# Optimization experiments

Measured on AMD Instinct MI355X. Metric: run time of the kernel, lower is better.

The kernel has to match this reference:

```python
import jax, jax.numpy as jnp
import numpy as np

K = 16
D_MODEL = 128

def _gather(pts, idx):
    # pts: [B,N,C], idx: [B,N,K] -> [B,N,K,C]
    return jax.vmap(lambda p, i: p[i])(pts, idx)

def setup_inputs() -> dict:
    key = jax.random.key(0)
    ks = jax.random.split(key, 20)
    s = 0.05
    def w(k_, shape):
        return jax.random.normal(k_, shape, dtype=jnp.float32) * s
    B, N, C = 4, 4096, 3
    TF, D = 128, D_MODEL
    return {
        "xyz": jax.random.normal(ks[0], (B, N, C), dtype=jnp.float32),
        "W0a": w(ks[1], (C, TF)),  "b0a": jnp.zeros((TF,), jnp.float32),
        "W0b": w(ks[2], (TF, TF)), "b0b": jnp.zeros((TF,), jnp.float32),
        "W1":  w(ks[3], (TF, D)),  "b1":  jnp.zeros((D,), jnp.float32),
        "W2":  w(ks[4], (D, TF)),  "b2":  jnp.zeros((TF,), jnp.float32),
        "Wd1": w(ks[5], (C, D)),   "bd1": jnp.zeros((D,), jnp.float32),
        "Wd2": w(ks[6], (D, D)),   "bd2": jnp.zeros((D,), jnp.float32),
        "Wg1": w(ks[7], (D, D)),   "bg1": jnp.zeros((D,), jnp.float32),
        "Wg2": w(ks[8], (D, D)),   "bg2": jnp.zeros((D,), jnp.float32),
        "Wq":  w(ks[9], (D, D)),
        "Wk":  w(ks[10], (D, D)),
        "Wv":  w(ks[11], (D, D)),
    }

def reference(xyz, W0a, b0a, W0b, b0b, W1, b1, W2, b2,
              Wd1, bd1, Wd2, bd2, Wg1, bg1, Wg2, bg2, Wq, Wk, Wv):
    sq = jnp.sum(xyz * xyz, axis=-1)
    dists = sq[:, :, None] - 2.0 * jnp.einsum('bnc,bmc->bnm', xyz, xyz) + sq[:, None, :]
    _, knn_idx = jax.lax.top_k(-dists, K)          # [B,N,K] nearest neighbors

    knn_xyz = _gather(xyz, knn_idx)                # [B,N,K,3]
    features = jax.nn.relu(xyz @ W0a + b0a) @ W0b + b0b   # fc0  [B,N,TF]
    pre = features
    x = features @ W1 + b1                          # fc1  [B,N,D]
    q = x @ Wq                                      # [B,N,D]
    kf = _gather(x @ Wk, knn_idx)                   # [B,N,K,D]
    vf = _gather(x @ Wv, knn_idx)                   # [B,N,K,D]

    delta = xyz[:, :, None, :] - knn_xyz            # [B,N,K,3]
    pos_enc = jax.nn.relu(delta @ Wd1 + bd1) @ Wd2 + bd2   # fc_delta [B,N,K,D]

    h = q[:, :, None, :] - kf + pos_enc
    attn_logits = jax.nn.relu(h @ Wg1 + bg1) @ Wg2 + bg2   # fc_gamma [B,N,K,D]
    attn = jax.nn.softmax(attn_logits / np.sqrt(D_MODEL).astype(np.float32), axis=-2)

    res = jnp.einsum('bmnf,bmnf->bmf', attn, vf + pos_enc)  # [B,N,D]
    res = res @ W2 + b2 + pre                               # [B,N,TF]
    return res, attn
```

## Files before the change

kernel.cpp:

```cpp
#include <hip/hip_runtime.h>
#include <math.h>

#define BB 4
#define NN 4096
#define KNNK 16
#define DD 128
#define BN (BB*NN)

typedef __attribute__((ext_vector_type(8))) short short8;
typedef __attribute__((ext_vector_type(4))) float floatx4;

__device__ __forceinline__ short f2bf(float x) {
  unsigned u = __float_as_uint(x);
  unsigned r = (u + 0x7fffu + ((u >> 16) & 1u)) >> 16;
  return (short)r;
}

__device__ __forceinline__ float bf2f(short h) {
  return __uint_as_float((unsigned)(unsigned short)h << 16);
}

__device__ __forceinline__ void split_from_lds(const float* __restrict__ trans,
                                               int c, int g, short8 ah[4],
                                               short8 al[4]) {
#pragma unroll
  for (int s = 0; s < 4; ++s) {
    const float* p_ = &trans[c * 132 + s * 32 + g * 8];
    float4 u0 = *reinterpret_cast<const float4*>(p_);
    float4 u1 = *reinterpret_cast<const float4*>(p_ + 4);
    float tmp[8] = {u0.x, u0.y, u0.z, u0.w, u1.x, u1.y, u1.z, u1.w};
#pragma unroll
    for (int j = 0; j < 8; ++j) {
      short h_ = f2bf(tmp[j]);
      ah[s][j] = h_;
      al[s][j] = f2bf(tmp[j] - bf2f(h_));
    }
  }
}

__device__ __forceinline__ void split_gemm2(const short* __restrict__ Bh,
                                            int nt0, int lane,
                                            const short8 ah[4],
                                            const short8 al[4], floatx4& acc0,
                                            floatx4& acc1) {
  const short* Bl = Bh + 16384;
#pragma unroll
  for (int ks = 0; ks < 4; ++ks) {
    const size_t o0 = ((size_t)((nt0 + 0) * 4 + ks) * 64 + lane) * 8;
    const size_t o1 = ((size_t)((nt0 + 1) * 4 + ks) * 64 + lane) * 8;
    short8 bh0 = *reinterpret_cast<const short8*>(Bh + o0);
    short8 bl0 = *reinterpret_cast<const short8*>(Bl + o0);
    short8 bh1 = *reinterpret_cast<const short8*>(Bh + o1);
    short8 bl1 = *reinterpret_cast<const short8*>(Bl + o1);
    acc0 = __builtin_amdgcn_mfma_f32_16x16x32_bf16(ah[ks], bh0, acc0, 0, 0, 0);
    acc1 = __builtin_amdgcn_mfma_f32_16x16x32_bf16(ah[ks], bh1, acc1, 0, 0, 0);
    acc0 = __builtin_amdgcn_mfma_f32_16x16x32_bf16(ah[ks], bl0, acc0, 0, 0, 0);
    acc1 = __builtin_amdgcn_mfma_f32_16x16x32_bf16(ah[ks], bl1, acc1, 0, 0, 0);
    acc0 = __builtin_amdgcn_mfma_f32_16x16x32_bf16(al[ks], bh0, acc0, 0, 0, 0);
    acc1 = __builtin_amdgcn_mfma_f32_16x16x32_bf16(al[ks], bh1, acc1, 0, 0, 0);
  }
}

__device__ __forceinline__ void ced(double& a, double& b) {
  double mn = fmin(a, b);
  double mx = fmax(a, b);
  a = mn;
  b = mx;
}

__device__ __forceinline__ void dsort16(double v[16]) {
#define CE(i, j) ced(v[i], v[j]);
  CE(0, 1) CE(2, 3) CE(4, 5) CE(6, 7) CE(8, 9) CE(10, 11) CE(12, 13) CE(14, 15)
  CE(0, 2) CE(1, 3) CE(4, 6) CE(5, 7) CE(8, 10) CE(9, 11) CE(12, 14) CE(13, 15)
  CE(1, 2) CE(5, 6) CE(9, 10) CE(13, 14)
  CE(0, 4) CE(1, 5) CE(2, 6) CE(3, 7) CE(8, 12) CE(9, 13) CE(10, 14) CE(11, 15)
  CE(2, 4) CE(3, 5) CE(10, 12) CE(11, 13)
  CE(1, 2) CE(3, 4) CE(5, 6) CE(9, 10) CE(11, 12) CE(13, 14)
  CE(0, 8) CE(1, 9) CE(2, 10) CE(3, 11) CE(4, 12) CE(5, 13) CE(6, 14) CE(7, 15)
  CE(4, 8) CE(5, 9) CE(6, 10) CE(7, 11)
  CE(2, 4) CE(3, 5) CE(6, 8) CE(7, 9) CE(10, 12) CE(11, 13)
  CE(1, 2) CE(3, 4) CE(5, 6) CE(7, 8) CE(9, 10) CE(11, 12) CE(13, 14)
#undef CE
}

__device__ __forceinline__ void dbitonic16(double m[16]) {
#pragma unroll
  for (int s = 8; s >= 1; s >>= 1) {
#pragma unroll
    for (int i = 0; i < 16; ++i) {
      if ((i & s) == 0) ced(m[i], m[i + s]);
    }
  }
}

__global__ __launch_bounds__(256, 4) void knn_kernel(const float* __restrict__ xyz,
                                                     int* __restrict__ knn) {
  const int wv = threadIdx.x >> 6;
  const int lane = threadIdx.x & 63;
  const int q = blockIdx.x * 4 + wv;
  const int b = q >> 12;
  const int n = q & 4095;
  const float* xb = xyz + (size_t)b * NN * 3;

  const float qx = xb[n * 3 + 0], qy = xb[n * 3 + 1], qz = xb[n * 3 + 2];
  const float qsq = __fadd_rn(__fadd_rn(__fmul_rn(qx, qx), __fmul_rn(qy, qy)),
                              __fmul_rn(qz, qz));

  double top[16];
#pragma unroll
  for (int batch = 0; batch < 4; ++batch) {
    double v[16];
#pragma unroll
    for (int i = 0; i < 16; ++i) {
      const int c = (batch * 16 + i) * 64 + lane;
      float cx = xb[c * 3 + 0], cy = xb[c * 3 + 1], cz = xb[c * 3 + 2];
      float csq = __fadd_rn(__fadd_rn(__fmul_rn(cx, cx), __fmul_rn(cy, cy)),
                            __fmul_rn(cz, cz));
      float dot = __fadd_rn(__fadd_rn(__fmul_rn(qx, cx), __fmul_rn(qy, cy)),
                            __fmul_rn(qz, cz));
      float d = __fadd_rn(__fsub_rn(qsq, __fmul_rn(2.0f, dot)), csq);
      unsigned u = __float_as_uint(d);
      u = (u & 0x80000000u) ? ~u : (u | 0x80000000u);
      unsigned long long key =
          0x3FF0000000000000ULL | (((unsigned long long)u << 12) | (unsigned)c);
      v[i] = __longlong_as_double((long long)key);
    }
    dsort16(v);
    if (batch == 0) {
#pragma unroll
      for (int i = 0; i < 16; ++i) top[i] = v[i];
    } else {
      double m[16];
#pragma unroll
      for (int i = 0; i < 16; ++i)
        m[i] = fmin(top[i], v[15 - i]);
      dbitonic16(m);
#pragma unroll
      for (int i = 0; i < 16; ++i) top[i] = m[i];
    }
  }

#pragma unroll
  for (int mask = 1; mask <= 32; mask <<= 1) {
    double oth[16];
#pragma unroll
    for (int i = 0; i < 16; ++i) {
      double y = __shfl_xor(top[15 - i], mask);
      oth[i] = fmin(y, top[i]);
    }
    dbitonic16(oth);
#pragma unroll
    for (int i = 0; i < 16; ++i) top[i] = oth[i];
  }

  if (lane == 0) {
    int* outp = knn + (size_t)q * KNNK;
#pragma unroll
    for (int k = 0; k < 16; ++k)
      outp[k] = (int)(__double_as_longlong(top[k]) & 0xFFFLL);
  }
}

__global__ void swz_all_kernel(const float* __restrict__ Wd2,
                               const float* __restrict__ Wg1,
                               const float* __restrict__ Wg2,
                               const float* __restrict__ W0b,
                               const float* __restrict__ W1,
                               const float* __restrict__ Wq,
                               const float* __restrict__ Wk,
                               const float* __restrict__ Wv,
                               const float* __restrict__ W2,
                               short* __restrict__ wsw,
                               short* __restrict__ wsplit) {
  int t = blockIdx.x * 256 + threadIdx.x;
  if (t < 3 * 2048) {
    int stage = t / 2048;
    int rem = t % 2048;
    int nt = rem / 256;
    int ks = (rem % 256) / 64;
    int lane = rem % 64;
    const float* W = (stage == 0) ? Wd2 : (stage == 1) ? Wg1 : Wg2;
    short8 o;
#pragma unroll
    for (int j = 0; j < 8; ++j) {
      int k = ks * 32 + (lane >> 4) * 8 + j;
      int n = nt * 16 + (lane & 15);
      o[j] = f2bf(W[k * 128 + n]);
    }
    *reinterpret_cast<short8*>(wsw + (size_t)t * 8) = o;
  } else {
    int u = t - 3 * 2048;
    if (u >= 6 * 2048) return;
    int mat = u / 2048;
    int rem = u % 2048;
    int nt = rem / 256;
    int ks = (rem % 256) / 64;
    int lane = rem % 64;
    const float* W = (mat == 0) ? W0b : (mat == 1) ? W1 : (mat == 2) ? Wq
                     : (mat == 3) ? Wk : (mat == 4) ? Wv : W2;
    short8 hi, lo;
#pragma unroll
    for (int j = 0; j < 8; ++j) {
      int k = ks * 32 + (lane >> 4) * 8 + j;
      int n = nt * 16 + (lane & 15);
      float w = W[k * 128 + n];
      short h = f2bf(w);
      hi[j] = h;
      lo[j] = f2bf(w - bf2f(h));
    }
    *reinterpret_cast<short8*>(wsplit + ((size_t)(2 * mat) * 2048 + rem) * 8) = hi;
    *reinterpret_cast<short8*>(wsplit + ((size_t)(2 * mat + 1) * 2048 + rem) * 8) = lo;
  }
}

__global__ __launch_bounds__(256, 4) void point_mlp_mfma_kernel(
    const float* __restrict__ xyz, const float* __restrict__ W0a,
    const float* __restrict__ b0a, const float* __restrict__ b0b,
    const float* __restrict__ b1, const short* __restrict__ wsplit,
    float* __restrict__ pre, float* __restrict__ qv, float* __restrict__ kv,
    float* __restrict__ vv) {
  const int wv = threadIdx.x >> 6;
  const int lane = threadIdx.x & 63;
  const int g = lane >> 4;
  const int c = lane & 15;
  const int g0 = blockIdx.x * 16;
  const int nt0 = wv * 2;

  __shared__ __attribute__((aligned(16))) float trans[16 * 132];
  __shared__ float xs[64];
  if (threadIdx.x < 48) {
    int p = threadIdx.x / 3, cc = threadIdx.x % 3;
    xs[p * 4 + cc] = xyz[(size_t)(g0 + p) * 3 + cc];
  }
  __syncthreads();

  short8 ah[4], al[4];
  {
    const float x0 = xs[c * 4 + 0], x1 = xs[c * 4 + 1], x2 = xs[c * 4 + 2];
#pragma unroll
    for (int s = 0; s < 4; ++s) {
#pragma unroll
      for (int j = 0; j < 8; ++j) {
        const int k = s * 32 + g * 8 + j;
        float v = fmaf(x2, W0a[256 + k],
                       fmaf(x1, W0a[128 + k], fmaf(x0, W0a[k], b0a[k])));
        v = fmaxf(v, 0.f);
        const short h = f2bf(v);
        ah[s][j] = h;
        al[s][j] = f2bf(v - bf2f(h));
      }
    }
  }

  floatx4 acc0, acc1;
  const floatx4 zf = (floatx4){0.f, 0.f, 0.f, 0.f};

  acc0 = zf; acc1 = zf;
  split_gemm2(wsplit + 0 * 32768, nt0, lane, ah, al, acc0, acc1);
  {
    const float bb0 = b0b[nt0 * 16 + c];
    const float bb1 = b0b[(nt0 + 1) * 16 + c];
#pragma unroll
    for (int r = 0; r < 4; ++r) {
      const int row = g * 4 + r;
      float v0 = acc0[r] + bb0;
      float v1 = acc1[r] + bb1;
      pre[(size_t)(g0 + row) * 128 + nt0 * 16 + c] = v0;
      pre[(size_t)(g0 + row) * 128 + (nt0 + 1) * 16 + c] = v1;
      trans[row * 132 + nt0 * 16 + c] = v0;
      trans[row * 132 + (nt0 + 1) * 16 + c] = v1;
    }
  }
  __syncthreads();
  split_from_lds(trans, c, g, ah, al);
  __syncthreads();

  acc0 = zf; acc1 = zf;
  split_gemm2(wsplit + 1 * 32768, nt0, lane, ah, al, acc0, acc1);
  {
    const float bb0 = b1[nt0 * 16 + c];
    const float bb1 = b1[(nt0 + 1) * 16 + c];
#pragma unroll
    for (int r = 0; r < 4; ++r) {
      const int row = g * 4 + r;
      trans[row * 132 + nt0 * 16 + c] = acc0[r] + bb0;
      trans[row * 132 + (nt0 + 1) * 16 + c] = acc1[r] + bb1;
    }
  }
  __syncthreads();
  split_from_lds(trans, c, g, ah, al);
  __syncthreads();

#define GSTORE(dst)                                                            \
  _Pragma("unroll") for (int r = 0; r < 4; ++r) {                              \
    const int row = g0 + g * 4 + r;                                            \
    dst[(size_t)row * 128 + nt0 * 16 + c] = acc0[r];                           \
    dst[(size_t)row * 128 + (nt0 + 1) * 16 + c] = acc1[r];                     \
  }

  acc0 = zf; acc1 = zf;
  split_gemm2(wsplit + 2 * 32768, nt0, lane, ah, al, acc0, acc1);
  GSTORE(qv);

  acc0 = zf; acc1 = zf;
  split_gemm2(wsplit + 3 * 32768, nt0, lane, ah, al, acc0, acc1);
  GSTORE(kv);

  acc0 = zf; acc1 = zf;
  split_gemm2(wsplit + 4 * 32768, nt0, lane, ah, al, acc0, acc1);
  GSTORE(vv);

#undef GSTORE
}

__global__ __launch_bounds__(256, 4) void attn_mfma_kernel(
    const float* __restrict__ xyz, const int* __restrict__ knn,
    const float* __restrict__ qv, const float* __restrict__ kv,
    const float* __restrict__ vv, const short* __restrict__ wsw,
    const float* __restrict__ Wd1, const float* __restrict__ bd1,
    const float* __restrict__ bd2, const float* __restrict__ bg1,
    const float* __restrict__ bg2, float* __restrict__ res_ws,
    float* __restrict__ out_attn) {
  const int wv = threadIdx.x >> 6;
  const int lane = threadIdx.x & 63;
  const int g = lane >> 4;
  const int c = lane & 15;
  const int bn = blockIdx.x * 4 + wv;
  const int b = bn >> 12;
  const int base_n = b << 12;

  __shared__ __attribute__((aligned(16))) short conv[4][16 * 136];

  const int* knnp = knn + (size_t)bn * 16;
  const int idxn = knnp[c];
  int idxr[4];
#pragma unroll
  for (int r = 0; r < 4; ++r) idxr[r] = knnp[g * 4 + r];

  float kvf[8][4];
#pragma unroll
  for (int nt = 0; nt < 8; ++nt)
#pragma unroll
    for (int r = 0; r < 4; ++r)
      kvf[nt][r] = kv[((size_t)(base_n + idxr[r])) * 128 + nt * 16 + c];

  const float ddx = xyz[(size_t)bn * 3 + 0] - xyz[((size_t)(base_n + idxn)) * 3 + 0];
  const float ddy = xyz[(size_t)bn * 3 + 1] - xyz[((size_t)(base_n + idxn)) * 3 + 1];
  const float ddz = xyz[(size_t)bn * 3 + 2] - xyz[((size_t)(base_n + idxn)) * 3 + 2];

  short8 af[4];
#pragma unroll
  for (int s = 0; s < 4; ++s) {
#pragma unroll
    for (int j = 0; j < 8; ++j) {
      int d = s * 32 + g * 8 + j;
      float v = fmaf(ddz, Wd1[256 + d],
                     fmaf(ddy, Wd1[128 + d], fmaf(ddx, Wd1[d], bd1[d])));
      af[s][j] = f2bf(fmaxf(v, 0.f));
    }
  }

  float qc[8], bd2v[8];
#pragma unroll
  for (int nt = 0; nt < 8; ++nt) {
    qc[nt] = qv[(size_t)bn * 128 + nt * 16 + c];
    bd2v[nt] = bd2[nt * 16 + c];
  }

  floatx4 acc[8];

#pragma unroll
  for (int nt = 0; nt < 8; ++nt) acc[nt] = (floatx4){0.f, 0.f, 0.f, 0.f};
  {
    const short* Wst = wsw;
#pragma unroll
    for (int ks = 0; ks < 4; ++ks) {
#pragma unroll
      for (int nt = 0; nt < 8; ++nt) {
        short8 bf = *reinterpret_cast<const short8*>(
            Wst + ((size_t)(nt * 4 + ks) * 64 + lane) * 8);
        acc[nt] = __builtin_amdgcn_mfma_f32_16x16x32_bf16(af[ks], bf, acc[nt],
                                                          0, 0, 0);
      }
    }
  }

  float PE[8][4];
#pragma unroll
  for (int nt = 0; nt < 8; ++nt) {
#pragma unroll
    for (int r = 0; r < 4; ++r) {
      float pe = acc[nt][r] + bd2v[nt];
      PE[nt][r] = pe;
      conv[wv][(g * 4 + r) * 136 + nt * 16 + c] =
          f2bf(qc[nt] - kvf[nt][r] + pe);
    }
  }
  __syncthreads();
#pragma unroll
  for (int s = 0; s < 4; ++s)
    af[s] = *reinterpret_cast<const short8*>(&conv[wv][c * 136 + s * 32 + g * 8]);
  __syncthreads();

#pragma unroll
  for (int nt = 0; nt < 8; ++nt) acc[nt] = (floatx4){0.f, 0.f, 0.f, 0.f};
  {
    const short* Wst = wsw + 16384;
#pragma unroll
    for (int ks = 0; ks < 4; ++ks) {
#pragma unroll
      for (int nt = 0; nt < 8; ++nt) {
        short8 bf = *reinterpret_cast<const short8*>(
            Wst + ((size_t)(nt * 4 + ks) * 64 + lane) * 8);
        acc[nt] = __builtin_amdgcn_mfma_f32_16x16x32_bf16(af[ks], bf, acc[nt],
                                                          0, 0, 0);
      }
    }
  }
#pragma unroll
  for (int nt = 0; nt < 8; ++nt) {
    const float bg1v = bg1[nt * 16 + c];
#pragma unroll
    for (int r = 0; r < 4; ++r) {
      conv[wv][(g * 4 + r) * 136 + nt * 16 + c] =
          f2bf(fmaxf(acc[nt][r] + bg1v, 0.f));
    }
  }
  __syncthreads();
#pragma unroll
  for (int s = 0; s < 4; ++s)
    af[s] = *reinterpret_cast<const short8*>(&conv[wv][c * 136 + s * 32 + g * 8]);
  __syncthreads();

#pragma unroll
  for (int nt = 0; nt < 8; ++nt) acc[nt] = (floatx4){0.f, 0.f, 0.f, 0.f};
  {
    const short* Wst = wsw + 32768;
#pragma unroll
    for (int ks = 0; ks < 4; ++ks) {
#pragma unroll
      for (int nt = 0; nt < 8; ++nt) {
        short8 bf = *reinterpret_cast<const short8*>(
            Wst + ((size_t)(nt * 4 + ks) * 64 + lane) * 8);
        acc[nt] = __builtin_amdgcn_mfma_f32_16x16x32_bf16(af[ks], bf, acc[nt],
                                                          0, 0, 0);
      }
    }
  }

  const float inv = 0.0883883476483184f;
  float resv[8];
#pragma unroll
  for (int nt = 0; nt < 8; ++nt) {
    const float bg2v = bg2[nt * 16 + c];
    float l0 = (acc[nt][0] + bg2v) * inv;
    float l1 = (acc[nt][1] + bg2v) * inv;
    float l2 = (acc[nt][2] + bg2v) * inv;
    float l3 = (acc[nt][3] + bg2v) * inv;
    float m4 = fmaxf(fmaxf(l0, l1), fmaxf(l2, l3));
    m4 = fmaxf(m4, __shfl_xor(m4, 16));
    m4 = fmaxf(m4, __shfl_xor(m4, 32));
    float e0 = expf(l0 - m4), e1 = expf(l1 - m4);
    float e2 = expf(l2 - m4), e3 = expf(l3 - m4);
    float s4 = e0 + e1 + e2 + e3;
    s4 += __shfl_xor(s4, 16);
    s4 += __shfl_xor(s4, 32);
    float rs = 1.f / s4;
    float a0 = e0 * rs, a1 = e1 * rs, a2 = e2 * rs, a3 = e3 * rs;
    size_t base = ((size_t)bn * 16 + g * 4) * 128 + nt * 16 + c;
    out_attn[base + 0 * 128] = a0;
    out_attn[base + 1 * 128] = a1;
    out_attn[base + 2 * 128] = a2;
    out_attn[base + 3 * 128] = a3;
    float r = 0.f;
    {
      float v0 = vv[((size_t)(base_n + idxr[0])) * 128 + nt * 16 + c];
      float v1 = vv[((size_t)(base_n + idxr[1])) * 128 + nt * 16 + c];
      float v2 = vv[((size_t)(base_n + idxr[2])) * 128 + nt * 16 + c];
      float v3 = vv[((size_t)(base_n + idxr[3])) * 128 + nt * 16 + c];
      r = fmaf(a0, v0 + PE[nt][0], r);
      r = fmaf(a1, v1 + PE[nt][1], r);
      r = fmaf(a2, v2 + PE[nt][2], r);
      r = fmaf(a3, v3 + PE[nt][3], r);
    }
    r += __shfl_xor(r, 16);
    r += __shfl_xor(r, 32);
    resv[nt] = r;
  }
  if (g == 0) {
#pragma unroll
    for (int nt = 0; nt < 8; ++nt)
      res_ws[(size_t)bn * 128 + nt * 16 + c] = resv[nt];
  }
}

__global__ __launch_bounds__(256, 4) void epilogue_mfma_kernel(
    const float* __restrict__ res_ws, const short* __restrict__ wsplit,
    const float* __restrict__ b2, const float* __restrict__ pre,
    float* __restrict__ out_res) {
  const int wv = threadIdx.x >> 6;
  const int lane = threadIdx.x & 63;
  const int g = lane >> 4;
  const int c = lane & 15;
  const int g0 = blockIdx.x * 16;
  const int nt0 = wv * 2;

  __shared__ __attribute__((aligned(16))) float trans[16 * 132];

#pragma unroll
  for (int i = 0; i < 2; ++i) {
    int idx4 = threadIdx.x + i * 256;
    int row = idx4 >> 5;
    int col4 = idx4 & 31;
    float4 v = *reinterpret_cast<const float4*>(
        res_ws + (size_t)(g0 + row) * 128 + col4 * 4);
    *reinterpret_cast<float4*>(&trans[row * 132 + col4 * 4]) = v;
  }
  __syncthreads();

  short8 ah[4], al[4];
  split_from_lds(trans, c, g, ah, al);

  float prv0[4], prv1[4];
  const float bb0 = b2[nt0 * 16 + c];
  const float bb1 = b2[(nt0 + 1) * 16 + c];
#pragma unroll
  for (int r = 0; r < 4; ++r) {
    prv0[r] = pre[(size_t)(g0 + g * 4 + r) * 128 + nt0 * 16 + c];
    prv1[r] = pre[(size_t)(g0 + g * 4 + r) * 128 + (nt0 + 1) * 16 + c];
  }

  floatx4 acc0 = (floatx4){0.f, 0.f, 0.f, 0.f};
  floatx4 acc1 = (floatx4){0.f, 0.f, 0.f, 0.f};
  split_gemm2(wsplit + 5 * 32768, nt0, lane, ah, al, acc0, acc1);

#pragma unroll
  for (int r = 0; r < 4; ++r) {
    const int row = g0 + g * 4 + r;
    out_res[(size_t)row * 128 + nt0 * 16 + c] = acc0[r] + bb0 + prv0[r];
    out_res[(size_t)row * 128 + (nt0 + 1) * 16 + c] = acc1[r] + bb1 + prv1[r];
  }
}

extern "C" void kernel_launch(void* const* d_in, const int* in_sizes, int n_in,
                              void* d_out, int out_size, void* d_ws,
                              size_t ws_size, hipStream_t stream) {
  const float* xyz = (const float*)d_in[0];
  const float* W0a = (const float*)d_in[1];
  const float* b0a = (const float*)d_in[2];
  const float* W0b = (const float*)d_in[3];
  const float* b0b = (const float*)d_in[4];
  const float* W1 = (const float*)d_in[5];
  const float* b1 = (const float*)d_in[6];
  const float* W2 = (const float*)d_in[7];
  const float* b2 = (const float*)d_in[8];
  const float* Wd1 = (const float*)d_in[9];
  const float* bd1 = (const float*)d_in[10];
  const float* Wd2 = (const float*)d_in[11];
  const float* bd2 = (const float*)d_in[12];
  const float* Wg1 = (const float*)d_in[13];
  const float* bg1 = (const float*)d_in[14];
  const float* Wg2 = (const float*)d_in[15];
  const float* bg2 = (const float*)d_in[16];
  const float* Wq = (const float*)d_in[17];
  const float* Wk = (const float*)d_in[18];
  const float* Wv = (const float*)d_in[19];

  char* ws = (char*)d_ws;
  int* knn = (int*)ws;
  float* pre = (float*)(ws + (1 << 20));
  float* qv = (float*)(ws + (9 << 20));
  float* kv = (float*)(ws + (17 << 20));
  float* vv = (float*)(ws + (25 << 20));
  float* res_ws = (float*)(ws + (33 << 20));
  short* wsw = (short*)(ws + (41 << 20));
  short* wsplit = (short*)(ws + (41 << 20) + (128 << 10));

  float* out_res = (float*)d_out;
  float* out_attn = out_res + (size_t)BN * DD;

  hipLaunchKernelGGL(swz_all_kernel, dim3(72), dim3(256), 0, stream, Wd2, Wg1,
                     Wg2, W0b, W1, Wq, Wk, Wv, W2, wsw, wsplit);
  hipLaunchKernelGGL(knn_kernel, dim3(4096), dim3(256), 0, stream, xyz, knn);
  hipLaunchKernelGGL(point_mlp_mfma_kernel, dim3(1024), dim3(256), 0, stream,
                     xyz, W0a, b0a, b0b, b1, wsplit, pre, qv, kv, vv);
  hipLaunchKernelGGL(attn_mfma_kernel, dim3(4096), dim3(256), 0, stream, xyz,
                     knn, qv, kv, vv, wsw, Wd1, bd1, bd2, bg1, bg2, res_ws,
                     out_attn);
  hipLaunchKernelGGL(epilogue_mfma_kernel, dim3(1024), dim3(256), 0, stream,
                     res_ws, wsplit, b2, pre, out_res);
}
```

Baseline: 381.0 us.

## Replace block barriers with per-wave LDS fences and batch weight loads in MFMA stages

Swaps the __syncthreads around the per-wave conv staging buffer for an lgkmcnt wait, since each wave only touches its own LDS slice. Groups the B-fragment loads four at a time ahead of the MFMAs in each GEMM stage. Splits the last GEMM and softmax into two halves, prefetching the gathered V values before the MFMAs so global latency overlaps compute. The aim is to cut block-wide stalls and expose more memory-level parallelism. In return it leans on the assumption that the LDS regions are wave-private, and it raises register pressure.

```diff
diff --git a/kernel.cpp b/kernel.cpp
--- a/kernel.cpp
+++ b/kernel.cpp
@@ -19,6 +19,8 @@
 __device__ __forceinline__ float bf2f(short h) {
   return __uint_as_float((unsigned)(unsigned short)h << 16);
 }
+
+#define LDSFENCE() asm volatile("s_waitcnt lgkmcnt(0)" ::: "memory")
 
 __device__ __forceinline__ void split_from_lds(const float* __restrict__ trans,
                                                int c, int g, short8 ah[4],
@@ -369,21 +371,25 @@
 
   floatx4 acc[8];
 
+#define STAGE_GEMM(WOFF)                                                       \
+  {                                                                            \
+    const short* Wst = wsw + (WOFF);                                           \
+    _Pragma("unroll") for (int ks = 0; ks < 4; ++ks) {                         \
+      _Pragma("unroll") for (int h2 = 0; h2 < 2; ++h2) {                       \
+        short8 bfr[4];                                                         \
+        _Pragma("unroll") for (int i = 0; i < 4; ++i)                          \
+          bfr[i] = *reinterpret_cast<const short8*>(                           \
+              Wst + ((size_t)((h2 * 4 + i) * 4 + ks) * 64 + lane) * 8);        \
+        _Pragma("unroll") for (int i = 0; i < 4; ++i)                          \
+          acc[h2 * 4 + i] = __builtin_amdgcn_mfma_f32_16x16x32_bf16(           \
+              af[ks], bfr[i], acc[h2 * 4 + i], 0, 0, 0);                       \
+      }                                                                        \
+    }                                                                          \
+  }
+
 #pragma unroll
   for (int nt = 0; nt < 8; ++nt) acc[nt] = (floatx4){0.f, 0.f, 0.f, 0.f};
-  {
-    const short* Wst = wsw;
-#pragma unroll
-    for (int ks = 0; ks < 4; ++ks) {
-#pragma unroll
-      for (int nt = 0; nt < 8; ++nt) {
-        short8 bf = *reinterpret_cast<const short8*>(
-            Wst + ((size_t)(nt * 4 + ks) * 64 + lane) * 8);
-        acc[nt] = __builtin_amdgcn_mfma_f32_16x16x32_bf16(af[ks], bf, acc[nt],
-                                                          0, 0, 0);
-      }
-    }
-  }
+  STAGE_GEMM(0);
 
   float PE[8][4];
 #pragma unroll
@@ -396,27 +402,14 @@
           f2bf(qc[nt] - kvf[nt][r] + pe);
     }
   }
-  __syncthreads();
+  LDSFENCE();
 #pragma unroll
   for (int s = 0; s < 4; ++s)
     af[s] = *reinterpret_cast<const short8*>(&conv[wv][c * 136 + s * 32 + g * 8]);
-  __syncthreads();
 
 #pragma unroll
   for (int nt = 0; nt < 8; ++nt) acc[nt] = (floatx4){0.f, 0.f, 0.f, 0.f};
-  {
-    const short* Wst = wsw + 16384;
-#pragma unroll
-    for (int ks = 0; ks < 4; ++ks) {
-#pragma unroll
-      for (int nt = 0; nt < 8; ++nt) {
-        short8 bf = *reinterpret_cast<const short8*>(
-            Wst + ((size_t)(nt * 4 + ks) * 64 + lane) * 8);
-        acc[nt] = __builtin_amdgcn_mfma_f32_16x16x32_bf16(af[ks], bf, acc[nt],
-                                                          0, 0, 0);
-      }
-    }
-  }
+  STAGE_GEMM(16384);
 #pragma unroll
   for (int nt = 0; nt < 8; ++nt) {
     const float bg1v = bg1[nt * 16 + c];
@@ -426,67 +419,78 @@
           f2bf(fmaxf(acc[nt][r] + bg1v, 0.f));
     }
   }
-  __syncthreads();
+  LDSFENCE();
 #pragma unroll
   for (int s = 0; s < 4; ++s)
     af[s] = *reinterpret_cast<const short8*>(&conv[wv][c * 136 + s * 32 + g * 8]);
-  __syncthreads();
-
-#pragma unroll
-  for (int nt = 0; nt < 8; ++nt) acc[nt] = (floatx4){0.f, 0.f, 0.f, 0.f};
-  {
-    const short* Wst = wsw + 32768;
-#pragma unroll
-    for (int ks = 0; ks < 4; ++ks) {
-#pragma unroll
-      for (int nt = 0; nt < 8; ++nt) {
-        short8 bf = *reinterpret_cast<const short8*>(
-            Wst + ((size_t)(nt * 4 + ks) * 64 + lane) * 8);
-        acc[nt] = __builtin_amdgcn_mfma_f32_16x16x32_bf16(af[ks], bf, acc[nt],
-                                                          0, 0, 0);
-      }
-    }
-  }
 
   const float inv = 0.0883883476483184f;
   float resv[8];
 #pragma unroll
-  for (int nt = 0; nt < 8; ++nt) {
-    const float bg2v = bg2[nt * 16 + c];
-    float l0 = (acc[nt][0] + bg2v) * inv;
-    float l1 = (acc[nt][1] + bg2v) * inv;
-    float l2 = (acc[nt][2] + bg2v) * inv;
-    float l3 = (acc[nt][3] + bg2v) * inv;
-    float m4 = fmaxf(fmaxf(l0, l1), fmaxf(l2, l3));
-    m4 = fmaxf(m4, __shfl_xor(m4, 16));
-    m4 = fmaxf(m4, __shfl_xor(m4, 32));
-    float e0 = expf(l0 - m4), e1 = expf(l1 - m4);
-    float e2 = expf(l2 - m4), e3 = expf(l3 - m4);
-    float s4 = e0 + e1 + e2 + e3;
-    s4 += __shfl_xor(s4, 16);
-    s4 += __shfl_xor(s4, 32);
-    float rs = 1.f / s4;
-    float a0 = e0 * rs, a1 = e1 * rs, a2 = e2 * rs, a3 = e3 * rs;
-    size_t base = ((size_t)bn * 16 + g * 4) * 128 + nt * 16 + c;
-    out_attn[base + 0 * 128] = a0;
-    out_attn[base + 1 * 128] = a1;
-    out_attn[base + 2 * 128] = a2;
-    out_attn[base + 3 * 128] = a3;
-    float r = 0.f;
+  for (int h = 0; h < 2; ++h) {
+    const int ntb = h * 4;
+    float vvf[4][4];
+#pragma unroll
+    for (int i = 0; i < 4; ++i)
+#pragma unroll
+      for (int r = 0; r < 4; ++r)
+        vvf[i][r] =
+            vv[((size_t)(base_n + idxr[r])) * 128 + (ntb + i) * 16 + c];
+
+    floatx4 acch[4];
+#pragma unroll
+    for (int i = 0; i < 4; ++i) acch[i] = (floatx4){0.f, 0.f, 0.f, 0.f};
     {
-      float v0 = vv[((size_t)(base_n + idxr[0])) * 128 + nt * 16 + c];
-      float v1 = vv[((size_t)(base_n + idxr[1])) * 128 + nt * 16 + c];
-      float v2 = vv[((size_t)(base_n + idxr[2])) * 128 + nt * 16 + c];
-      float v3 = vv[((size_t)(base_n + idxr[3])) * 128 + nt * 16 + c];
-      r = fmaf(a0, v0 + PE[nt][0], r);
-      r = fmaf(a1, v1 + PE[nt][1], r);
-      r = fmaf(a2, v2 + PE[nt][2], r);
-      r = fmaf(a3, v3 + PE[nt][3], r);
-    }
-    r += __shfl_xor(r, 16);
-    r += __shfl_xor(r, 32);
-    resv[nt] = r;
-  }
+      const short* Wst = wsw + 32768;
+#pragma unroll
+      for (int ks = 0; ks < 4; ++ks) {
+        short8 bfr[4];
+#pragma unroll
+        for (int i = 0; i < 4; ++i)
+          bfr[i] = *reinterpret_cast<const short8*>(
+              Wst + ((size_t)((ntb + i) * 4 + ks) * 64 + lane) * 8);
+#pragma unroll
+        for (int i = 0; i < 4; ++i)
+          acch[i] = __builtin_amdgcn_mfma_f32_16x16x32_bf16(af[ks], bfr[i],
+                                                            acch[i], 0, 0, 0);
+      }
+    }
+
+#pragma unroll
+    for (int i = 0; i < 4; ++i) {
+      const int nt = ntb + i;
+      const float bg2v = bg2[nt * 16 + c];
+      float l0 = (acch[i][0] + bg2v) * inv;
+      float l1 = (acch[i][1] + bg2v) * inv;
+      float l2 = (acch[i][2] + bg2v) * inv;
+      float l3 = (acch[i][3] + bg2v) * inv;
+      float m4 = fmaxf(fmaxf(l0, l1), fmaxf(l2, l3));
+      m4 = fmaxf(m4, __shfl_xor(m4, 16));
+      m4 = fmaxf(m4, __shfl_xor(m4, 32));
+      float e0 = expf(l0 - m4), e1 = expf(l1 - m4);
+      float e2 = expf(l2 - m4), e3 = expf(l3 - m4);
+      float s4 = e0 + e1 + e2 + e3;
+      s4 += __shfl_xor(s4, 16);
+      s4 += __shfl_xor(s4, 32);
+      float rs = 1.f / s4;
+      float a0 = e0 * rs, a1 = e1 * rs, a2 = e2 * rs, a3 = e3 * rs;
+      size_t base = ((size_t)bn * 16 + g * 4) * 128 + nt * 16 + c;
+      out_attn[base + 0 * 128] = a0;
+      out_attn[base + 1 * 128] = a1;
+      out_attn[base + 2 * 128] = a2;
+      out_attn[base + 3 * 128] = a3;
+      float r = 0.f;
+      r = fmaf(a0, vvf[i][0] + PE[nt][0], r);
+      r = fmaf(a1, vvf[i][1] + PE[nt][1], r);
+      r = fmaf(a2, vvf[i][2] + PE[nt][2], r);
+      r = fmaf(a3, vvf[i][3] + PE[nt][3], r);
+      r += __shfl_xor(r, 16);
+      r += __shfl_xor(r, 32);
+      resv[nt] = r;
+    }
+  }
+#undef STAGE_GEMM
+
   if (g == 0) {
 #pragma unroll
     for (int nt = 0; nt < 8; ++nt)
```

After: 373.3 us. -2.0%, faster.
